# Kernel optimization log

Hardware: AMD Instinct MI355X
Metric: run time of the kernel (lower is better)

The kernel has to match this reference:

```python
import jax, jax.numpy as jnp
import numpy as np

D_MODEL = 1024
N_HEADS = 16
D_K = 64
D_V = 64
NEG = -1e9
EPS = 1e-6


def setup_inputs() -> dict:
    key = jax.random.key(0)
    ks = jax.random.split(key, 7)
    B, L = 8, 1024
    X = jax.random.normal(ks[0], (B, L, D_MODEL), dtype=jnp.float32)
    attn_mask = jax.random.randint(ks[1], (B, 1, L, L), 0, 2) == 1  # True = masked
    s = 1.0 / np.sqrt(D_MODEL)
    W_Q = jax.random.normal(ks[2], (D_MODEL, N_HEADS * D_K), dtype=jnp.float32) * s
    W_K = jax.random.normal(ks[3], (D_MODEL, N_HEADS * D_K), dtype=jnp.float32) * s
    W_V = jax.random.normal(ks[4], (D_MODEL, N_HEADS * D_V), dtype=jnp.float32) * s
    W_O = jax.random.normal(ks[5], (N_HEADS * D_V, D_MODEL), dtype=jnp.float32) * (1.0 / np.sqrt(N_HEADS * D_V))
    gamma = jnp.ones((D_MODEL,), dtype=jnp.float32)
    beta = jnp.zeros((D_MODEL,), dtype=jnp.float32)
    return {"X": X, "attn_mask": attn_mask, "W_Q": W_Q, "W_K": W_K,
            "W_V": W_V, "W_O": W_O, "gamma": gamma, "beta": beta}


def _layer_norm(x, gamma, beta):
    mu = jnp.mean(x, axis=-1, keepdims=True)
    var = jnp.mean(jnp.square(x - mu), axis=-1, keepdims=True)
    return (x - mu) * jax.lax.rsqrt(var + EPS) * gamma + beta


def reference(X, attn_mask, W_Q, W_K, W_V, W_O, gamma, beta):
    B, L, _ = X.shape
    # project and split heads: [B, H, L, d]
    Q = (X @ W_Q).reshape(B, L, N_HEADS, D_K).transpose(0, 2, 1, 3)
    K = (X @ W_K).reshape(B, L, N_HEADS, D_K).transpose(0, 2, 1, 3)
    V = (X @ W_V).reshape(B, L, N_HEADS, D_V).transpose(0, 2, 1, 3)
    scale = 1.0 / np.sqrt(D_K)
    scores = jnp.einsum('bhqd,bhkd->bhqk', Q, K) * scale  # [B,H,L,L]
    scores = jnp.where(attn_mask, NEG, scores)
    attn = jax.nn.softmax(scores, axis=-1)
    context = jnp.einsum('bhqk,bhkd->bhqd', attn, V)  # [B,H,L,d_v]
    context = context.transpose(0, 2, 1, 3).reshape(B, L, N_HEADS * D_V)
    output = context @ W_O
    return _layer_norm(output + X, gamma, beta), attn
```

## Files before the change

### kernel.cpp

```cpp
#include <hip/hip_runtime.h>
#include <cstdint>


#define WS_XB   0u
#define WS_WT   16777216u
#define WS_WOT  (WS_WT + 6291456u)
#define WS_M8   (WS_WOT + 2097152u)
#define WS_Q    (WS_M8 + 8388608u)
#define WS_K    (WS_Q + 16777216u)
#define WS_V    (WS_K + 16777216u)

typedef short v8s __attribute__((ext_vector_type(8)));
typedef float v4f __attribute__((ext_vector_type(4)));

__device__ __forceinline__ short bf16rn(float f) {
  uint32_t u = __builtin_bit_cast(uint32_t, f);
  u += 0x7fffu + ((u >> 16) & 1u);
  return (short)(u >> 16);
}
__device__ __forceinline__ float bf2f(uint16_t h) {
  uint32_t u = ((uint32_t)h) << 16;
  return __builtin_bit_cast(float, u);
}
__device__ __forceinline__ v4f mfma16(v8s a, v8s b, v4f c) {
  return __builtin_amdgcn_mfma_f32_16x16x32_bf16(a, b, c, 0, 0, 0);
}
__device__ __forceinline__ void gload16(const short* g, short* l) {
  __builtin_amdgcn_global_load_lds(
      (const __attribute__((address_space(1))) unsigned int*)g,
      (__attribute__((address_space(3))) unsigned int*)l, 16, 0, 0);
}

__global__ void k_cvt_x(const float* __restrict__ X, short* __restrict__ Xb) {
  int i = (blockIdx.x * 256 + threadIdx.x) * 4;
  float4 v = *(const float4*)(X + i);
  short4 o;
  o.x = bf16rn(v.x); o.y = bf16rn(v.y); o.z = bf16rn(v.z); o.w = bf16rn(v.w);
  *(short4*)(Xb + i) = o;
}

__global__ void k_tw(const float* __restrict__ WQ, const float* __restrict__ WK,
                     const float* __restrict__ WV, const float* __restrict__ WO,
                     short* __restrict__ Wt, short* __restrict__ WOt) {
  __shared__ float tile[32][33];
  int k0 = blockIdx.x * 32, n0 = blockIdx.y * 32;
  int tx = threadIdx.x, ty = threadIdx.y;
  const float* src; short* dst; int nloc, drow;
  if (n0 < 3072) {
    int wsel = n0 >> 10;
    src = wsel == 0 ? WQ : (wsel == 1 ? WK : WV);
    nloc = n0 & 1023; dst = Wt; drow = n0;
  } else {
    src = WO; nloc = n0 - 3072; dst = WOt; drow = n0 - 3072;
  }
#pragma unroll
  for (int i = 0; i < 4; ++i)
    tile[ty + 8 * i][tx] = src[(size_t)(k0 + ty + 8 * i) * 1024 + nloc + tx];
  __syncthreads();
#pragma unroll
  for (int i = 0; i < 4; ++i)
    dst[(size_t)(drow + ty + 8 * i) * 1024 + k0 + tx] = bf16rn(tile[tx][ty + 8 * i]);
}

__global__ void k_msk(const int* __restrict__ M, uint32_t* __restrict__ M8) {
  int i = blockIdx.x * 256 + threadIdx.x;
  int4 v = *(const int4*)(M + (size_t)i * 4);
  uint32_t u = (uint32_t)(v.x != 0) | ((uint32_t)(v.y != 0) << 8) |
               ((uint32_t)(v.z != 0) << 16) | ((uint32_t)(v.w != 0) << 24);
  M8[i] = u;
}

template <int MODE>
__global__ __launch_bounds__(256) void k_gemm(const short* __restrict__ A,
                                              const short* __restrict__ Bt,
                                              short* __restrict__ Q, short* __restrict__ Kp,
                                              short* __restrict__ V,
                                              const float* __restrict__ Xres,
                                              float* __restrict__ Y) {
  __shared__ short As[128 * 32];
  __shared__ short Bs[128 * 32];
  const int nwg = gridDim.x * gridDim.y;
  const int id = blockIdx.y * gridDim.x + blockIdx.x;
  const int swz = (id & 7) * (nwg >> 3) + (id >> 3);
  const int bx = swz % gridDim.x, by = swz / gridDim.x;
  const int m0 = by * 128, n0 = bx * 128;
  const int t = threadIdx.x, w = t >> 6, lane = t & 63, col = lane & 15, quad = lane >> 4;
  const int wm = w >> 1, wn = w & 1;
  const v4f vz = {0.f, 0.f, 0.f, 0.f};
  v4f acc[4][4];
#pragma unroll
  for (int i = 0; i < 4; ++i)
#pragma unroll
    for (int j = 0; j < 4; ++j) acc[i][j] = vz;

  const int srow = lane >> 2, sseg = lane & 3;
  const short* ga = A + (size_t)(m0 + w * 32 + srow) * 1024 + sseg * 8;
  const short* gb = Bt + (size_t)(n0 + w * 32 + srow) * 1024 + sseg * 8;
  short* la = As + (w * 32) * 32;
  short* lb = Bs + (w * 32) * 32;

  for (int kc = 0; kc < 32; ++kc) {
    __syncthreads();
    gload16(ga + kc * 32, la);
    gload16(ga + kc * 32 + 16 * 1024, la + 16 * 32);
    gload16(gb + kc * 32, lb);
    gload16(gb + kc * 32 + 16 * 1024, lb + 16 * 32);
    __syncthreads();
    v8s af[4], bf[4];
#pragma unroll
    for (int i = 0; i < 4; ++i) {
      af[i] = *(const v8s*)(As + (wm * 64 + i * 16 + col) * 32 + quad * 8);
      bf[i] = *(const v8s*)(Bs + (wn * 64 + i * 16 + col) * 32 + quad * 8);
    }
#pragma unroll
    for (int mi = 0; mi < 4; ++mi)
#pragma unroll
      for (int ni = 0; ni < 4; ++ni)
        acc[mi][ni] = mfma16(af[mi], bf[ni], acc[mi][ni]);
  }

  if (MODE == 0) {
    const int which = n0 >> 10;
    if (which == 2) {
#pragma unroll
      for (int mi = 0; mi < 4; ++mi)
#pragma unroll
        for (int ni = 0; ni < 4; ++ni) {
          int n = n0 + wn * 64 + ni * 16 + col;
          int h = (n >> 6) & 15, d = n & 63;
          int mbase = m0 + wm * 64 + mi * 16 + quad * 4;
          int b = mbase >> 10, l = mbase & 1023;
          short4 pk;
          pk.x = bf16rn(acc[mi][ni][0]); pk.y = bf16rn(acc[mi][ni][1]);
          pk.z = bf16rn(acc[mi][ni][2]); pk.w = bf16rn(acc[mi][ni][3]);
          *(short4*)(V + ((size_t)((b * 16 + h) * 64 + d)) * 1024 + l) = pk;
        }
    } else {
      short* dst = which == 0 ? Q : Kp;
      const float qs = which == 0 ? 0.125f : 1.0f;
#pragma unroll
      for (int mi = 0; mi < 4; ++mi)
#pragma unroll
        for (int ni = 0; ni < 4; ++ni) {
          int n = n0 + wn * 64 + ni * 16 + col;
          int h = (n >> 6) & 15, d = n & 63;
          int mbase = m0 + wm * 64 + mi * 16 + quad * 4;
#pragma unroll
          for (int rg = 0; rg < 4; ++rg) {
            int m = mbase + rg, b = m >> 10, l = m & 1023;
            dst[((size_t)((b * 16 + h) * 1024 + l)) * 64 + d] = bf16rn(acc[mi][ni][rg] * qs);
          }
        }
    }
  } else {
#pragma unroll
    for (int mi = 0; mi < 4; ++mi)
#pragma unroll
      for (int ni = 0; ni < 4; ++ni) {
        int n = n0 + wn * 64 + ni * 16 + col;
        int mbase = m0 + wm * 64 + mi * 16 + quad * 4;
#pragma unroll
        for (int rg = 0; rg < 4; ++rg) {
          int m = mbase + rg;
          Y[(size_t)m * 1024 + n] = acc[mi][ni][rg] + Xres[(size_t)m * 1024 + n];
        }
      }
  }
}

__global__ __launch_bounds__(256) void k_attn(const short* __restrict__ Qb,
                                              const short* __restrict__ Kb,
                                              const short* __restrict__ Vt,
                                              const uint8_t* __restrict__ M8,
                                              float* __restrict__ attn,
                                              short* __restrict__ ctxb) {
  __shared__ short Pb[32 * 136];
  __shared__ float red[4][32];
  __shared__ float fin[32];

  const int lid = blockIdx.y * 32 + blockIdx.x;
  const int swz = (lid & 7) * 512 + (lid >> 3);
  const int bh = swz >> 5, q0 = (swz & 31) * 32, b = bh >> 4, h = bh & 15;
  const int t = threadIdx.x, w = t >> 6, lane = t & 63, col = lane & 15, quad = lane >> 4;
  const v4f vz = {0.f, 0.f, 0.f, 0.f};

  v8s qf[2][2];
#pragma unroll
  for (int qt = 0; qt < 2; ++qt)
#pragma unroll
    for (int dh2 = 0; dh2 < 2; ++dh2)
      qf[qt][dh2] = *(const v8s*)(Qb + ((size_t)bh * 1024 + q0 + qt * 16 + col) * 64 + dh2 * 32 + quad * 8);

  const size_t kvbase = (size_t)bh * 1024;
  float lrun[2] = {0.f, 0.f};

  for (int s = 0; s < 8; ++s) {
#pragma unroll
    for (int kt = 0; kt < 2; ++kt) {
      int kr0 = w * 32 + kt * 16;
      const short* grow = Kb + (kvbase + s * 128 + kr0 + col) * 64;
      v8s a0 = *(const v8s*)(grow + quad * 8);
      v8s a1 = *(const v8s*)(grow + 32 + quad * 8);
#pragma unroll
      for (int qt = 0; qt < 2; ++qt) {
        v4f c = vz;
        c = mfma16(a0, qf[qt][0], c);
        c = mfma16(a1, qf[qt][1], c);
        int q = q0 + qt * 16 + col;
        uint32_t mu = *(const uint32_t*)(M8 + ((size_t)b * 1024 + q) * 1024 + s * 128 + kr0 + quad * 4);
        float es = 0.f;
#pragma unroll
        for (int rg = 0; rg < 4; ++rg)
          if (!((mu >> (8 * rg)) & 0xffu)) es += __expf(c[rg]);
        es += __shfl_xor(es, 16);
        es += __shfl_xor(es, 32);
        lrun[qt] += es;
      }
    }
  }
  if (quad == 0) {
    red[w][col] = lrun[0];
    red[w][16 + col] = lrun[1];
  }
  __syncthreads();
  if (t < 32) {
    float Lx = red[0][t] + red[1][t] + red[2][t] + red[3][t];
    fin[t] = Lx > 0.f ? 1.f / Lx : 0.f;
  }
  __syncthreads();
  float Rq[2];
  Rq[0] = fin[col]; Rq[1] = fin[16 + col];

  const int qh = w & 1, dh = w >> 1;
  v4f ctx[2] = {vz, vz};

  for (int s = 0; s < 8; ++s) {
#pragma unroll
    for (int kt = 0; kt < 2; ++kt) {
      int kr0 = w * 32 + kt * 16;
      const short* grow = Kb + (kvbase + s * 128 + kr0 + col) * 64;
      v8s a0 = *(const v8s*)(grow + quad * 8);
      v8s a1 = *(const v8s*)(grow + 32 + quad * 8);
#pragma unroll
      for (int qt = 0; qt < 2; ++qt) {
        v4f c = vz;
        c = mfma16(a0, qf[qt][0], c);
        c = mfma16(a1, qf[qt][1], c);
        int q = q0 + qt * 16 + col;
        uint32_t mu = *(const uint32_t*)(M8 + ((size_t)b * 1024 + q) * 1024 + s * 128 + kr0 + quad * 4);
        float p[4];
#pragma unroll
        for (int rg = 0; rg < 4; ++rg)
          p[rg] = ((mu >> (8 * rg)) & 0xffu) ? 0.f : __expf(c[rg]) * Rq[qt];
        uint32_t u01 = (uint32_t)(uint16_t)bf16rn(p[0]) | ((uint32_t)(uint16_t)bf16rn(p[1]) << 16);
        uint32_t u23 = (uint32_t)(uint16_t)bf16rn(p[2]) | ((uint32_t)(uint16_t)bf16rn(p[3]) << 16);
        int ql = qt * 16 + col;
        *(uint32_t*)(Pb + ql * 136 + kr0 + quad * 4) = u01;
        *(uint32_t*)(Pb + ql * 136 + kr0 + quad * 4 + 2) = u23;
      }
    }
    __syncthreads();
    {
      int q = t >> 3, j = t & 7;
      float* arow = attn + ((size_t)bh * 1024 + q0 + q) * 1024 + s * 128;
#pragma unroll
      for (int i = 0; i < 4; ++i) {
        const uint32_t* pp = (const uint32_t*)(Pb + q * 136 + j * 4 + i * 32);
        uint32_t p0 = pp[0], p1 = pp[1];
        float4 o;
        o.x = bf2f((uint16_t)p0); o.y = bf2f((uint16_t)(p0 >> 16));
        o.z = bf2f((uint16_t)p1); o.w = bf2f((uint16_t)(p1 >> 16));
        *(float4*)(arow + j * 4 + i * 32) = o;
      }
    }
#pragma unroll
    for (int kc = 0; kc < 128; kc += 32) {
      v8s pa = *(const v8s*)(Pb + (qh * 16 + col) * 136 + kc + quad * 8);
#pragma unroll
      for (int dt = 0; dt < 2; ++dt) {
        int d = dh * 32 + dt * 16 + col;
        v8s vb = *(const v8s*)(Vt + ((size_t)bh * 64 + d) * 1024 + s * 128 + kc + quad * 8);
        ctx[dt] = mfma16(pa, vb, ctx[dt]);
      }
    }
    __syncthreads();
  }
#pragma unroll
  for (int dt = 0; dt < 2; ++dt)
#pragma unroll
    for (int rg = 0; rg < 4; ++rg) {
      int q = q0 + qh * 16 + quad * 4 + rg;
      int d = dh * 32 + dt * 16 + col;
      ctxb[((size_t)(b * 1024 + q)) * 1024 + h * 64 + d] = bf16rn(ctx[dt][rg]);
    }
}

__global__ __launch_bounds__(256) void k_ln(const float* __restrict__ Y,
                                            const float* __restrict__ g,
                                            const float* __restrict__ be,
                                            float* __restrict__ out) {
  __shared__ float sred[4];
  const int row = blockIdx.x, t = threadIdx.x, w = t >> 6, lane = t & 63;
  const float4 v = *(const float4*)(Y + (size_t)row * 1024 + t * 4);
  float sum = v.x + v.y + v.z + v.w;
#pragma unroll
  for (int o = 32; o > 0; o >>= 1) sum += __shfl_down(sum, o);
  if (lane == 0) sred[w] = sum;
  __syncthreads();
  float mu = (sred[0] + sred[1] + sred[2] + sred[3]) * (1.f / 1024.f);
  float dx = v.x - mu, dy = v.y - mu, dz = v.z - mu, dw = v.w - mu;
  float sq = dx * dx + dy * dy + dz * dz + dw * dw;
#pragma unroll
  for (int o = 32; o > 0; o >>= 1) sq += __shfl_down(sq, o);
  __syncthreads();
  if (lane == 0) sred[w] = sq;
  __syncthreads();
  float var = (sred[0] + sred[1] + sred[2] + sred[3]) * (1.f / 1024.f);
  float rs = rsqrtf(var + 1e-6f);
  float4 gg = *(const float4*)(g + t * 4), bb = *(const float4*)(be + t * 4);
  float4 o4;
  o4.x = dx * rs * gg.x + bb.x;
  o4.y = dy * rs * gg.y + bb.y;
  o4.z = dz * rs * gg.z + bb.z;
  o4.w = dw * rs * gg.w + bb.w;
  *(float4*)(out + (size_t)row * 1024 + t * 4) = o4;
}

extern "C" void kernel_launch(void* const* d_in, const int* in_sizes, int n_in,
                              void* d_out, int out_size, void* d_ws, size_t ws_size,
                              hipStream_t stream) {
  const float* X  = (const float*)d_in[0];
  const int*   Mi = (const int*)d_in[1];
  const float* WQ = (const float*)d_in[2];
  const float* WK = (const float*)d_in[3];
  const float* WV = (const float*)d_in[4];
  const float* WO = (const float*)d_in[5];
  const float* g  = (const float*)d_in[6];
  const float* be = (const float*)d_in[7];

  char* ws = (char*)d_ws;
  short*    Xb  = (short*)(ws + WS_XB);
  short*    Wt  = (short*)(ws + WS_WT);
  short*    WOt = (short*)(ws + WS_WOT);
  uint8_t*  M8  = (uint8_t*)(ws + WS_M8);
  short*    Qb  = (short*)(ws + WS_Q);
  short*    Kb  = (short*)(ws + WS_K);
  short*    Vtb = (short*)(ws + WS_V);
  short*    Ctx = Xb;
  float*    Y   = (float*)(ws + WS_Q);

  float* out0 = (float*)d_out;
  float* attn = out0 + (size_t)8 * 1024 * 1024;

  k_cvt_x<<<8192, 256, 0, stream>>>(X, Xb);
  k_tw<<<dim3(32, 128), dim3(32, 8), 0, stream>>>(WQ, WK, WV, WO, Wt, WOt);
  k_msk<<<8192, 256, 0, stream>>>(Mi, (uint32_t*)M8);
  k_gemm<0><<<dim3(24, 64), 256, 0, stream>>>(Xb, Wt, Qb, Kb, Vtb, nullptr, nullptr);
  k_attn<<<dim3(32, 128), 256, 0, stream>>>(Qb, Kb, Vtb, M8, attn, Ctx);
  k_gemm<1><<<dim3(8, 64), 256, 0, stream>>>(Ctx, WOt, nullptr, nullptr, nullptr, X, Y);
  k_ln<<<8192, 256, 0, stream>>>(Y, g, be, out0);
}
```

Measured before the change: 1.051 ms.

## Bit-pack mask and cache unnormalized probabilities to skip second QK pass

The mask is packed to one bit per element with wave ballots instead of one byte, cutting mask read traffic in attention by 8x. The attention kernel now keeps the masked exp values as packed bf16 in registers from the first pass. The second pass rescales them instead of recomputing QK^T and exp and reloading K. Attention rows are written to global directly from each lane, which removes an LDS readback round trip. The cost is heavy register use (128 extra uint32 per thread), which may lower occupancy or spill, plus double bf16 rounding of the probabilities.

Measured after the change: 969.3 us. 7.8% less time.

```diff
diff --git a/kernel.cpp b/kernel.cpp
--- a/kernel.cpp
+++ b/kernel.cpp
@@ -17,6 +17,9 @@
   uint32_t u = __builtin_bit_cast(uint32_t, f);
   u += 0x7fffu + ((u >> 16) & 1u);
   return (short)(u >> 16);
+}
+__device__ __forceinline__ uint32_t bfpack(float a, float b) {
+  return (uint32_t)(uint16_t)bf16rn(a) | ((uint32_t)(uint16_t)bf16rn(b) << 16);
 }
 __device__ __forceinline__ float bf2f(uint16_t h) {
   uint32_t u = ((uint32_t)h) << 16;
@@ -62,12 +65,12 @@
     dst[(size_t)(drow + ty + 8 * i) * 1024 + k0 + tx] = bf16rn(tile[tx][ty + 8 * i]);
 }
 
-__global__ void k_msk(const int* __restrict__ M, uint32_t* __restrict__ M8) {
+__global__ void k_msk(const int* __restrict__ M, uint32_t* __restrict__ Mb) {
   int i = blockIdx.x * 256 + threadIdx.x;
-  int4 v = *(const int4*)(M + (size_t)i * 4);
-  uint32_t u = (uint32_t)(v.x != 0) | ((uint32_t)(v.y != 0) << 8) |
-               ((uint32_t)(v.z != 0) << 16) | ((uint32_t)(v.w != 0) << 24);
-  M8[i] = u;
+  unsigned long long bal = __ballot(M[i] != 0);
+  int lane = threadIdx.x & 63;
+  if (lane == 0)       Mb[i >> 5] = (uint32_t)bal;
+  else if (lane == 32) Mb[i >> 5] = (uint32_t)(bal >> 32);
 }
 
 template <int MODE>
@@ -171,7 +174,7 @@
 __global__ __launch_bounds__(256) void k_attn(const short* __restrict__ Qb,
                                               const short* __restrict__ Kb,
                                               const short* __restrict__ Vt,
-                                              const uint8_t* __restrict__ M8,
+                                              const uint32_t* __restrict__ Mb,
                                               float* __restrict__ attn,
                                               short* __restrict__ ctxb) {
   __shared__ short Pb[32 * 136];
@@ -192,35 +195,44 @@
       qf[qt][dh2] = *(const v8s*)(Qb + ((size_t)bh * 1024 + q0 + qt * 16 + col) * 64 + dh2 * 32 + quad * 8);
 
   const size_t kvbase = (size_t)bh * 1024;
-  float lrun[2] = {0.f, 0.f};
-
+  const short* gkw = Kb + (kvbase + w * 32 + col) * 64 + quad * 8;
+  const uint32_t* mrow0 = Mb + ((size_t)(b * 1024 + q0 + col)) * 32 + w;
+  const uint32_t* mrow1 = mrow0 + 16 * 32;
+
+  uint32_t pun[8][2][2][2];
+  float lr[2] = {0.f, 0.f};
+
+#pragma unroll
   for (int s = 0; s < 8; ++s) {
+    uint32_t mu0 = mrow0[s * 4], mu1 = mrow1[s * 4];
 #pragma unroll
     for (int kt = 0; kt < 2; ++kt) {
-      int kr0 = w * 32 + kt * 16;
-      const short* grow = Kb + (kvbase + s * 128 + kr0 + col) * 64;
-      v8s a0 = *(const v8s*)(grow + quad * 8);
-      v8s a1 = *(const v8s*)(grow + 32 + quad * 8);
+      const short* grow = gkw + (s * 128 + kt * 16) * 64;
+      v8s a0 = *(const v8s*)(grow);
+      v8s a1 = *(const v8s*)(grow + 32);
 #pragma unroll
       for (int qt = 0; qt < 2; ++qt) {
-        v4f c = vz;
-        c = mfma16(a0, qf[qt][0], c);
+        uint32_t mu = qt ? mu1 : mu0;
+        v4f c = mfma16(a0, qf[qt][0], vz);
         c = mfma16(a1, qf[qt][1], c);
-        int q = q0 + qt * 16 + col;
-        uint32_t mu = *(const uint32_t*)(M8 + ((size_t)b * 1024 + q) * 1024 + s * 128 + kr0 + quad * 4);
-        float es = 0.f;
-#pragma unroll
-        for (int rg = 0; rg < 4; ++rg)
-          if (!((mu >> (8 * rg)) & 0xffu)) es += __expf(c[rg]);
-        es += __shfl_xor(es, 16);
-        es += __shfl_xor(es, 32);
-        lrun[qt] += es;
+        const int sh = kt * 16 + quad * 4;
+        float e0 = ((mu >> (sh + 0)) & 1u) ? 0.f : __expf(c[0]);
+        float e1 = ((mu >> (sh + 1)) & 1u) ? 0.f : __expf(c[1]);
+        float e2 = ((mu >> (sh + 2)) & 1u) ? 0.f : __expf(c[2]);
+        float e3 = ((mu >> (sh + 3)) & 1u) ? 0.f : __expf(c[3]);
+        lr[qt] += (e0 + e1) + (e2 + e3);
+        pun[s][kt][qt][0] = bfpack(e0, e1);
+        pun[s][kt][qt][1] = bfpack(e2, e3);
       }
     }
   }
-  if (quad == 0) {
-    red[w][col] = lrun[0];
-    red[w][16 + col] = lrun[1];
+
+#pragma unroll
+  for (int qt = 0; qt < 2; ++qt) {
+    float es = lr[qt];
+    es += __shfl_xor(es, 16);
+    es += __shfl_xor(es, 32);
+    if (quad == 0) red[w][qt * 16 + col] = es;
   }
   __syncthreads();
   if (t < 32) {
@@ -234,45 +246,28 @@
   const int qh = w & 1, dh = w >> 1;
   v4f ctx[2] = {vz, vz};
 
+  float* arow0 = attn + ((size_t)bh * 1024 + q0 + col) * 1024 + w * 32 + quad * 4;
+  float* arow1 = arow0 + (size_t)16 * 1024;
+  short* pbr0 = Pb + col * 136 + w * 32 + quad * 4;
+  short* pbr1 = Pb + (16 + col) * 136 + w * 32 + quad * 4;
+#pragma unroll
   for (int s = 0; s < 8; ++s) {
 #pragma unroll
     for (int kt = 0; kt < 2; ++kt) {
-      int kr0 = w * 32 + kt * 16;
-      const short* grow = Kb + (kvbase + s * 128 + kr0 + col) * 64;
-      v8s a0 = *(const v8s*)(grow + quad * 8);
-      v8s a1 = *(const v8s*)(grow + 32 + quad * 8);
 #pragma unroll
       for (int qt = 0; qt < 2; ++qt) {
-        v4f c = vz;
-        c = mfma16(a0, qf[qt][0], c);
-        c = mfma16(a1, qf[qt][1], c);
-        int q = q0 + qt * 16 + col;
-        uint32_t mu = *(const uint32_t*)(M8 + ((size_t)b * 1024 + q) * 1024 + s * 128 + kr0 + quad * 4);
-        float p[4];
-#pragma unroll
-        for (int rg = 0; rg < 4; ++rg)
-          p[rg] = ((mu >> (8 * rg)) & 0xffu) ? 0.f : __expf(c[rg]) * Rq[qt];
-        uint32_t u01 = (uint32_t)(uint16_t)bf16rn(p[0]) | ((uint32_t)(uint16_t)bf16rn(p[1]) << 16);
-        uint32_t u23 = (uint32_t)(uint16_t)bf16rn(p[2]) | ((uint32_t)(uint16_t)bf16rn(p[3]) << 16);
-        int ql = qt * 16 + col;
-        *(uint32_t*)(Pb + ql * 136 + kr0 + quad * 4) = u01;
-        *(uint32_t*)(Pb + ql * 136 + kr0 + quad * 4 + 2) = u23;
+        uint32_t u01 = pun[s][kt][qt][0], u23 = pun[s][kt][qt][1];
+        float rq = qt ? Rq[1] : Rq[0];
+        float f0 = bf2f((uint16_t)u01) * rq, f1 = bf2f((uint16_t)(u01 >> 16)) * rq;
+        float f2 = bf2f((uint16_t)u23) * rq, f3 = bf2f((uint16_t)(u23 >> 16)) * rq;
+        float4 o = {f0, f1, f2, f3};
+        *(float4*)((qt ? arow1 : arow0) + s * 128 + kt * 16) = o;
+        short* pb = (qt ? pbr1 : pbr0) + kt * 16;
+        *(uint32_t*)pb = bfpack(f0, f1);
+        *(uint32_t*)(pb + 2) = bfpack(f2, f3);
       }
     }
     __syncthreads();
-    {
-      int q = t >> 3, j = t & 7;
-      float* arow = attn + ((size_t)bh * 1024 + q0 + q) * 1024 + s * 128;
-#pragma unroll
-      for (int i = 0; i < 4; ++i) {
-        const uint32_t* pp = (const uint32_t*)(Pb + q * 136 + j * 4 + i * 32);
-        uint32_t p0 = pp[0], p1 = pp[1];
-        float4 o;
-        o.x = bf2f((uint16_t)p0); o.y = bf2f((uint16_t)(p0 >> 16));
-        o.z = bf2f((uint16_t)p1); o.w = bf2f((uint16_t)(p1 >> 16));
-        *(float4*)(arow + j * 4 + i * 32) = o;
-      }
-    }
 #pragma unroll
     for (int kc = 0; kc < 128; kc += 32) {
       v8s pa = *(const v8s*)(Pb + (qh * 16 + col) * 136 + kc + quad * 8);
@@ -342,7 +337,7 @@
   short*    Xb  = (short*)(ws + WS_XB);
   short*    Wt  = (short*)(ws + WS_WT);
   short*    WOt = (short*)(ws + WS_WOT);
-  uint8_t*  M8  = (uint8_t*)(ws + WS_M8);
+  uint32_t* Mb  = (uint32_t*)(ws + WS_M8);
   short*    Qb  = (short*)(ws + WS_Q);
   short*    Kb  = (short*)(ws + WS_K);
   short*    Vtb = (short*)(ws + WS_V);
@@ -354,9 +349,9 @@
 
   k_cvt_x<<<8192, 256, 0, stream>>>(X, Xb);
   k_tw<<<dim3(32, 128), dim3(32, 8), 0, stream>>>(WQ, WK, WV, WO, Wt, WOt);
-  k_msk<<<8192, 256, 0, stream>>>(Mi, (uint32_t*)M8);
+  k_msk<<<32768, 256, 0, stream>>>(Mi, Mb);
   k_gemm<0><<<dim3(24, 64), 256, 0, stream>>>(Xb, Wt, Qb, Kb, Vtb, nullptr, nullptr);
-  k_attn<<<dim3(32, 128), 256, 0, stream>>>(Qb, Kb, Vtb, M8, attn, Ctx);
+  k_attn<<<dim3(32, 128), 256, 0, stream>>>(Qb, Kb, Vtb, Mb, attn, Ctx);
   k_gemm<1><<<dim3(8, 64), 256, 0, stream>>>(Ctx, WOt, nullptr, nullptr, nullptr, X, Y);
   k_ln<<<8192, 256, 0, stream>>>(Y, g, be, out0);
 }
```
